# Kernel optimization log

Hardware: AMD Instinct MI355X
Metric: run time of the kernel (lower is better)

The kernel has to match this reference:

```python
import jax, jax.numpy as jnp
import numpy as np

E = 8        # n_routed_experts
TOPK = 2     # num_experts_per_tok


def setup_inputs() -> dict:
    key = jax.random.key(0)
    k0, k1, k2, k3, k4 = jax.random.split(key, 5)
    B, S, D, H = 1, 2048, 1024, 2816
    scale = 0.02
    x = jax.random.normal(k0, (B, S, D), jnp.float32)
    Wg = jax.random.normal(k1, (E, D), jnp.float32) * scale   # gate weight [E, D]
    W1 = jax.random.normal(k2, (E, H, D), jnp.float32) * scale  # up-gate proj
    W2 = jax.random.normal(k3, (E, D, H), jnp.float32) * scale  # down proj
    W3 = jax.random.normal(k4, (E, H, D), jnp.float32) * scale  # up proj
    return {"x": x, "Wg": Wg, "W1": W1, "W2": W2, "W3": W3}


def _moe_forward(x, Wg, W1, W2, W3):
    B, S, D = x.shape
    xt = x.reshape(-1, D)                      # [T, D], T = B*S
    T = xt.shape[0]
    # --- gate: logits -> softmax -> top-k, normalized top-k weights ---
    logits = xt @ Wg.T                         # [T, E]
    scores = jax.nn.softmax(logits, axis=-1)
    w, idx = jax.lax.top_k(scores, TOPK)       # [T, K]
    w = w / (w.sum(axis=-1, keepdims=True) + 1e-20)
    # combine weights per token per expert (scatter top-k weights) [T, E]
    cw = jnp.zeros((T, E), xt.dtype).at[jnp.arange(T)[:, None], idx].add(w)
    # --- per-expert SwiGLU FFN (batched over experts) ---
    h = jax.nn.silu(jnp.einsum('td,ehd->teh', xt, W1)) * jnp.einsum('td,ehd->teh', xt, W3)  # [T,E,H]
    out = jnp.einsum('teh,edh->ted', h, W2)    # [T, E, D]
    # weighted combine of selected experts (cw is zero for unselected)
    y = jnp.einsum('te,ted->td', cw, out)      # [T, D]
    return y.reshape(B, S, D)


def reference(x, Wg, W1, W2, W3):
    return _moe_forward(x, Wg, W1, W2, W3)
```

## Files before the change

kernel.cpp:

```cpp
#include <hip/hip_runtime.h>
#include <hip/hip_bf16.h>

#define T_TOK 2048
#define D_DIM 1024
#define H_DIM 2816
#define E_NUM 8
#define CAP   1024

typedef __attribute__((ext_vector_type(8))) short short8;
typedef __attribute__((ext_vector_type(4))) float floatx4;

__device__ __forceinline__ unsigned short f2bf(float f) {
    unsigned int b = __float_as_uint(f);
    b += 0x7FFFu + ((b >> 16) & 1u);
    return (unsigned short)(b >> 16);
}

__device__ __forceinline__ unsigned pk2(float lo, float hi) {
    unsigned a = __float_as_uint(lo) + 0x8000u;
    unsigned b = __float_as_uint(hi) + 0x8000u;
    return __builtin_amdgcn_perm(b, a, 0x07060302);
}

__device__ __forceinline__ short8 pack8r(float4 a, float4 b) {
    union { uint4 u; short8 s; } r;
    r.u.x = pk2(a.x, a.y);
    r.u.y = pk2(a.z, a.w);
    r.u.z = pk2(b.x, b.y);
    r.u.w = pk2(b.z, b.w);
    return r.s;
}

__device__ __forceinline__ void gl2lds16(const void* g, void* l) {
    __builtin_amdgcn_global_load_lds(
        (const __attribute__((address_space(1))) unsigned int*)g,
        (__attribute__((address_space(3))) unsigned int*)l,
        16, 0, 0);
}


__global__ __launch_bounds__(256) void k_gate2(const float* __restrict__ x,
                                               const float* __restrict__ Wg,
                                               int* __restrict__ stok,
                                               float* __restrict__ sw,
                                               int* __restrict__ counts,
                                               unsigned short* __restrict__ xg) {
    const int wave = threadIdx.x >> 6, lane = threadIdx.x & 63;
    const int t = blockIdx.x * 4 + wave;
    const float* xr = x + (size_t)t * D_DIM;
    float acc[E_NUM];
#pragma unroll
    for (int e = 0; e < E_NUM; ++e) acc[e] = 0.f;
#pragma unroll 4
    for (int i = 0; i < D_DIM / 64; ++i) {
        float xv = xr[lane + 64 * i];
#pragma unroll
        for (int e = 0; e < E_NUM; ++e) acc[e] += xv * Wg[e * D_DIM + lane + 64 * i];
    }
#pragma unroll
    for (int e = 0; e < E_NUM; ++e) {
#pragma unroll
        for (int s = 32; s > 0; s >>= 1) acc[e] += __shfl_xor(acc[e], s, 64);
    }
    int slot0 = 0, slot1 = 0;
    if (lane == 0) {
        float mx = acc[0];
#pragma unroll
        for (int e = 1; e < E_NUM; ++e) mx = fmaxf(mx, acc[e]);
        float p[E_NUM], s = 0.f;
#pragma unroll
        for (int e = 0; e < E_NUM; ++e) { p[e] = __expf(acc[e] - mx); s += p[e]; }
        int i0 = 0;
#pragma unroll
        for (int e = 1; e < E_NUM; ++e) if (p[e] > p[i0]) i0 = e;
        int i1 = (i0 == 0) ? 1 : 0;
#pragma unroll
        for (int e = 0; e < E_NUM; ++e) if (e != i0 && p[e] > p[i1]) i1 = e;
        float s0 = p[i0] / s, s1 = p[i1] / s;
        float d = s0 + s1 + 1e-20f;
        int p0 = atomicAdd(&counts[i0], 1); if (p0 >= CAP) p0 = CAP - 1;
        int p1 = atomicAdd(&counts[i1], 1); if (p1 >= CAP) p1 = CAP - 1;
        slot0 = i0 * CAP + p0;
        slot1 = i1 * CAP + p1;
        stok[slot0] = t; sw[slot0] = s0 / d;
        stok[slot1] = t; sw[slot1] = s1 / d;
    }
    slot0 = __shfl(slot0, 0, 64);
    slot1 = __shfl(slot1, 0, 64);
    const float4* xr4 = (const float4*)xr;
    ushort4* xg4 = (ushort4*)xg;
#pragma unroll
    for (int it = 0; it < 4; ++it) {
        float4 v = xr4[lane + 64 * it];
        ushort4 o;
        o.x = f2bf(v.x); o.y = f2bf(v.y); o.z = f2bf(v.z); o.w = f2bf(v.w);
        xg4[(size_t)slot0 * 256 + lane + 64 * it] = o;
        xg4[(size_t)slot1 * 256 + lane + 64 * it] = o;
    }
}

__global__ __launch_bounds__(256, 2) void k_gemm13(const unsigned short* __restrict__ xg,
                                                   const float* __restrict__ W1,
                                                   const float* __restrict__ W3,
                                                   const int* __restrict__ counts,
                                                   unsigned short* __restrict__ U) {
    const int nt = blockIdx.x;
    const int mt = blockIdx.y;
    const int e  = blockIdx.z;
    const int cnt = min(counts[e], CAP);
    if (mt * 256 >= cnt) return;

    __shared__ __align__(16) unsigned char As[32768];
    __shared__ __align__(16) unsigned char B1s[4096];
    __shared__ __align__(16) unsigned char B3s[4096];

    const int tid = threadIdx.x, lane = tid & 63, wave = tid >> 6;
    const int fr = lane & 15, quad = lane >> 4, f7 = fr & 7, f8 = fr >> 3;

    const unsigned short* aBase = xg
        + ((size_t)e * CAP + mt * 256 + wave * 64 + (lane >> 3)) * D_DIM
        + ((lane & 7) ^ (lane >> 3)) * 8;

    const int br = tid >> 3, bc = tid & 7;
    const float* w1p = W1 + ((size_t)e * H_DIM + nt * 32 + br) * D_DIM + bc * 8;
    const float* w3p = W3 + ((size_t)e * H_DIM + nt * 32 + br) * D_DIM + bc * 8;
    const int bslot = (br >> 3) * 1024 + (br & 7) * 128 + ((bc ^ (br & 7)) << 4);

    floatx4 acc1[4][2], acc3[4][2];
#pragma unroll
    for (int m = 0; m < 4; ++m)
#pragma unroll
        for (int n = 0; n < 2; ++n) { acc1[m][n] = (floatx4)0.f; acc3[m][n] = (floatx4)0.f; }

    const int agrp = (wave * 8 + f8) * 1024 + f7 * 128;
    const int c0 = (quad ^ f7) << 4;
    const int c1 = ((4 | quad) ^ f7) << 4;

#pragma unroll
    for (int j = 0; j < 8; ++j)
        gl2lds16(aBase + (size_t)j * 8 * D_DIM, As + (wave * 8 + j) * 1024);
    {
        float4 u0 = *(const float4*)(w1p);
        float4 u1 = *(const float4*)(w1p + 4);
        float4 v0 = *(const float4*)(w3p);
        float4 v1 = *(const float4*)(w3p + 4);
        *(short8*)(B1s + bslot) = pack8r(u0, u1);
        *(short8*)(B3s + bslot) = pack8r(v0, v1);
    }
    __syncthreads();

#pragma unroll 1
    for (int t = 0; t < D_DIM / 64; ++t) {
        short8 a[4][2], b1[2][2], b3[2][2];
#pragma unroll
        for (int m = 0; m < 4; ++m) {
            const unsigned char* ab = As + agrp + m * 2048;
            a[m][0] = *(const short8*)(ab + c0);
            a[m][1] = *(const short8*)(ab + c1);
        }
#pragma unroll
        for (int n = 0; n < 2; ++n) {
            const int bg = (n * 2 + f8) * 1024 + f7 * 128;
            b1[n][0] = *(const short8*)(B1s + bg + c0);
            b1[n][1] = *(const short8*)(B1s + bg + c1);
            b3[n][0] = *(const short8*)(B3s + bg + c0);
            b3[n][1] = *(const short8*)(B3s + bg + c1);
        }
        __syncthreads();

        const bool more = (t < D_DIM / 64 - 1);
        float4 u0, u1, v0, v1;
        if (more) {
            const int kn = (t + 1) * 64;
#pragma unroll
            for (int j = 0; j < 8; ++j)
                gl2lds16(aBase + (size_t)j * 8 * D_DIM + kn, As + (wave * 8 + j) * 1024);
            u0 = *(const float4*)(w1p + kn);
            u1 = *(const float4*)(w1p + kn + 4);
            v0 = *(const float4*)(w3p + kn);
            v1 = *(const float4*)(w3p + kn + 4);
        }

#pragma unroll
        for (int m = 0; m < 4; ++m) {
#pragma unroll
            for (int n = 0; n < 2; ++n) {
                acc1[m][n] = __builtin_amdgcn_mfma_f32_16x16x32_bf16(a[m][0], b1[n][0], acc1[m][n], 0, 0, 0);
                acc1[m][n] = __builtin_amdgcn_mfma_f32_16x16x32_bf16(a[m][1], b1[n][1], acc1[m][n], 0, 0, 0);
                acc3[m][n] = __builtin_amdgcn_mfma_f32_16x16x32_bf16(a[m][0], b3[n][0], acc3[m][n], 0, 0, 0);
                acc3[m][n] = __builtin_amdgcn_mfma_f32_16x16x32_bf16(a[m][1], b3[n][1], acc3[m][n], 0, 0, 0);
            }
        }

        if (more) {
            *(short8*)(B1s + bslot) = pack8r(u0, u1);
            *(short8*)(B3s + bslot) = pack8r(v0, v1);
            __syncthreads();
        }
    }

#pragma unroll
    for (int m = 0; m < 4; ++m) {
#pragma unroll
        for (int r = 0; r < 4; ++r) {
            int g = mt * 256 + wave * 64 + m * 16 + quad * 4 + r;
            if (g < cnt) {
                size_t rowb = ((size_t)e * CAP + g) * H_DIM + nt * 32;
#pragma unroll
                for (int n = 0; n < 2; ++n) {
                    float u1v = acc1[m][n][r], u3v = acc3[m][n][r];
                    float u = u1v / (1.f + __expf(-u1v)) * u3v;
                    U[rowb + n * 16 + fr] = f2bf(u);
                }
            }
        }
    }
}

__global__ __launch_bounds__(256, 2) void k_gemm2(const unsigned short* __restrict__ U,
                                                  const float* __restrict__ W2,
                                                  const int* __restrict__ counts,
                                                  const int* __restrict__ stok,
                                                  const float* __restrict__ sw,
                                                  float* __restrict__ y) {
    const int nt = blockIdx.x;
    const int mt = blockIdx.y;
    const int e  = blockIdx.z;
    const int cnt = min(counts[e], CAP);
    if (mt * 256 >= cnt) return;

    __shared__ __align__(16) unsigned char As[32768];
    __shared__ __align__(16) unsigned char Bs[8192];

    const int tid = threadIdx.x, lane = tid & 63, wave = tid >> 6;
    const int fr = lane & 15, quad = lane >> 4, f7 = fr & 7, f8 = fr >> 3;

    const unsigned short* aBase = U
        + ((size_t)e * CAP + mt * 256 + wave * 64 + (lane >> 3)) * H_DIM
        + ((lane & 7) ^ (lane >> 3)) * 8;

    const int br = tid >> 3, bc = tid & 7;
    const float* w2p0 = W2 + ((size_t)e * D_DIM + nt * 64 + br) * H_DIM + bc * 8;
    const float* w2p1 = w2p0 + (size_t)32 * H_DIM;
    const int bslot0 = (br >> 3) * 1024 + (br & 7) * 128 + ((bc ^ (br & 7)) << 4);
    const int bslot1 = bslot0 + 4096;

    floatx4 acc[4][4];
#pragma unroll
    for (int m = 0; m < 4; ++m)
#pragma unroll
        for (int n = 0; n < 4; ++n) acc[m][n] = (floatx4)0.f;

    const int agrp = (wave * 8 + f8) * 1024 + f7 * 128;
    const int c0 = (quad ^ f7) << 4;
    const int c1 = ((4 | quad) ^ f7) << 4;

#pragma unroll
    for (int j = 0; j < 8; ++j)
        gl2lds16(aBase + (size_t)j * 8 * H_DIM, As + (wave * 8 + j) * 1024);
    {
        float4 u0 = *(const float4*)(w2p0);
        float4 u1 = *(const float4*)(w2p0 + 4);
        float4 v0 = *(const float4*)(w2p1);
        float4 v1 = *(const float4*)(w2p1 + 4);
        *(short8*)(Bs + bslot0) = pack8r(u0, u1);
        *(short8*)(Bs + bslot1) = pack8r(v0, v1);
    }
    __syncthreads();

#pragma unroll 1
    for (int t = 0; t < H_DIM / 64; ++t) {
        short8 a[4][2], bf[4][2];
#pragma unroll
        for (int m = 0; m < 4; ++m) {
            const unsigned char* ab = As + agrp + m * 2048;
            a[m][0] = *(const short8*)(ab + c0);
            a[m][1] = *(const short8*)(ab + c1);
        }
#pragma unroll
        for (int n = 0; n < 4; ++n) {
            const int bg = (n * 2 + f8) * 1024 + f7 * 128;
            bf[n][0] = *(const short8*)(Bs + bg + c0);
            bf[n][1] = *(const short8*)(Bs + bg + c1);
        }
        __syncthreads();

        const bool more = (t < H_DIM / 64 - 1);
        float4 u0, u1, v0, v1;
        if (more) {
            const int kn = (t + 1) * 64;
#pragma unroll
            for (int j = 0; j < 8; ++j)
                gl2lds16(aBase + (size_t)j * 8 * H_DIM + kn, As + (wave * 8 + j) * 1024);
            u0 = *(const float4*)(w2p0 + kn);
            u1 = *(const float4*)(w2p0 + kn + 4);
            v0 = *(const float4*)(w2p1 + kn);
            v1 = *(const float4*)(w2p1 + kn + 4);
        }

#pragma unroll
        for (int m = 0; m < 4; ++m) {
#pragma unroll
            for (int n = 0; n < 4; ++n) {
                acc[m][n] = __builtin_amdgcn_mfma_f32_16x16x32_bf16(a[m][0], bf[n][0], acc[m][n], 0, 0, 0);
                acc[m][n] = __builtin_amdgcn_mfma_f32_16x16x32_bf16(a[m][1], bf[n][1], acc[m][n], 0, 0, 0);
            }
        }

        if (more) {
            *(short8*)(Bs + bslot0) = pack8r(u0, u1);
            *(short8*)(Bs + bslot1) = pack8r(v0, v1);
            __syncthreads();
        }
    }

#pragma unroll
    for (int m = 0; m < 4; ++m) {
#pragma unroll
        for (int r = 0; r < 4; ++r) {
            int g = mt * 256 + wave * 64 + m * 16 + quad * 4 + r;
            if (g < cnt) {
                int slot = e * CAP + g;
                int t = stok[slot];
                float w = sw[slot];
                float* yr = y + (size_t)t * D_DIM + nt * 64;
#pragma unroll
                for (int n = 0; n < 4; ++n)
                    atomicAdd(&yr[n * 16 + fr], w * acc[m][n][r]);
            }
        }
    }
}

static const size_t OFF_XG   = 0;
static const size_t OFF_U    = (size_t)E_NUM * CAP * D_DIM * 2;
static const size_t OFF_STOK = OFF_U + (size_t)E_NUM * CAP * H_DIM * 2;
static const size_t OFF_SW   = OFF_STOK + (size_t)E_NUM * CAP * 4;
static const size_t OFF_META = OFF_SW + (size_t)E_NUM * CAP * 4;

extern "C" void kernel_launch(void* const* d_in, const int* in_sizes, int n_in,
                              void* d_out, int out_size, void* d_ws, size_t ws_size,
                              hipStream_t stream) {
    const float* x  = (const float*)d_in[0];
    const float* Wg = (const float*)d_in[1];
    const float* W1 = (const float*)d_in[2];
    const float* W2 = (const float*)d_in[3];
    const float* W3 = (const float*)d_in[4];
    float* y = (float*)d_out;
    char* ws = (char*)d_ws;

    unsigned short* xg = (unsigned short*)(ws + OFF_XG);
    unsigned short* U  = (unsigned short*)(ws + OFF_U);
    int*   stok   = (int*)(ws + OFF_STOK);
    float* sw     = (float*)(ws + OFF_SW);
    int*   counts = (int*)(ws + OFF_META);

    hipMemsetAsync(counts, 0, 64, stream);
    hipMemsetAsync(y, 0, (size_t)T_TOK * D_DIM * sizeof(float), stream);

    k_gate2<<<T_TOK / 4, 256, 0, stream>>>(x, Wg, stok, sw, counts, xg);
    k_gemm13<<<dim3(H_DIM / 32, CAP / 256, E_NUM), 256, 0, stream>>>(xg, W1, W3, counts, U);
    k_gemm2<<<dim3(D_DIM / 64, CAP / 256, E_NUM), 256, 0, stream>>>(U, W2, counts, stok, sw, y);
}
```

Before: 431.2 us.

## Widen gate/up GEMM tile, split-K the down GEMM, reorder loads with sched barriers

The fused W1/W3 GEMM now computes 64 H-columns per block instead of 32, so each staged token tile is reused across twice as many output columns and the grid shrinks. The down-projection GEMM splits its H reduction into two halves across blocks, relying on the existing accumulate-into-y epilogue, to raise block count and parallelism. In both kernels the weight global loads for the next step are issued at the top of the iteration, fenced by sched_barrier, and the gemm13 MFMA work is split into two k-halves to overlap LDS reads with compute. The trade-offs are more accumulator registers and LDS in gemm13, which may hurt occupancy, and more atomic traffic to y from the split-K.

```diff
diff --git a/kernel.cpp b/kernel.cpp
--- a/kernel.cpp
+++ b/kernel.cpp
@@ -6,6 +6,9 @@
 #define H_DIM 2816
 #define E_NUM 8
 #define CAP   1024
+
+#define NT13  (D_DIM / 64)
+#define NT2H  (H_DIM / 128)
 
 typedef __attribute__((ext_vector_type(8))) short short8;
 typedef __attribute__((ext_vector_type(4))) float floatx4;
@@ -37,6 +40,8 @@
         (__attribute__((address_space(3))) unsigned int*)l,
         16, 0, 0);
 }
+
+#define SCHED0 __builtin_amdgcn_sched_barrier(0)
 
 
 __global__ __launch_bounds__(256) void k_gate2(const float* __restrict__ x,
@@ -111,8 +116,8 @@
     if (mt * 256 >= cnt) return;
 
     __shared__ __align__(16) unsigned char As[32768];
-    __shared__ __align__(16) unsigned char B1s[4096];
-    __shared__ __align__(16) unsigned char B3s[4096];
+    __shared__ __align__(16) unsigned char B1s[8192];
+    __shared__ __align__(16) unsigned char B3s[8192];
 
     const int tid = threadIdx.x, lane = tid & 63, wave = tid >> 6;
     const int fr = lane & 15, quad = lane >> 4, f7 = fr & 7, f8 = fr >> 3;
@@ -122,79 +127,111 @@
         + ((lane & 7) ^ (lane >> 3)) * 8;
 
     const int br = tid >> 3, bc = tid & 7;
-    const float* w1p = W1 + ((size_t)e * H_DIM + nt * 32 + br) * D_DIM + bc * 8;
-    const float* w3p = W3 + ((size_t)e * H_DIM + nt * 32 + br) * D_DIM + bc * 8;
+    const float* w1p = W1 + ((size_t)e * H_DIM + nt * 64 + br) * D_DIM + bc * 8;
+    const float* w3p = W3 + ((size_t)e * H_DIM + nt * 64 + br) * D_DIM + bc * 8;
     const int bslot = (br >> 3) * 1024 + (br & 7) * 128 + ((bc ^ (br & 7)) << 4);
 
-    floatx4 acc1[4][2], acc3[4][2];
+    floatx4 acc1[4][4], acc3[4][4];
 #pragma unroll
     for (int m = 0; m < 4; ++m)
 #pragma unroll
-        for (int n = 0; n < 2; ++n) { acc1[m][n] = (floatx4)0.f; acc3[m][n] = (floatx4)0.f; }
+        for (int n = 0; n < 4; ++n) { acc1[m][n] = (floatx4)0.f; acc3[m][n] = (floatx4)0.f; }
 
     const int agrp = (wave * 8 + f8) * 1024 + f7 * 128;
     const int c0 = (quad ^ f7) << 4;
     const int c1 = ((4 | quad) ^ f7) << 4;
 
-#pragma unroll
-    for (int j = 0; j < 8; ++j)
-        gl2lds16(aBase + (size_t)j * 8 * D_DIM, As + (wave * 8 + j) * 1024);
     {
         float4 u0 = *(const float4*)(w1p);
         float4 u1 = *(const float4*)(w1p + 4);
+        float4 u2 = *(const float4*)(w1p + (size_t)32 * D_DIM);
+        float4 u3 = *(const float4*)(w1p + (size_t)32 * D_DIM + 4);
         float4 v0 = *(const float4*)(w3p);
         float4 v1 = *(const float4*)(w3p + 4);
-        *(short8*)(B1s + bslot) = pack8r(u0, u1);
-        *(short8*)(B3s + bslot) = pack8r(v0, v1);
+        float4 v2 = *(const float4*)(w3p + (size_t)32 * D_DIM);
+        float4 v3 = *(const float4*)(w3p + (size_t)32 * D_DIM + 4);
+        SCHED0;
+#pragma unroll
+        for (int j = 0; j < 8; ++j)
+            gl2lds16(aBase + (size_t)j * 8 * D_DIM, As + (wave * 8 + j) * 1024);
+        SCHED0;
+        *(short8*)(B1s + bslot)        = pack8r(u0, u1);
+        *(short8*)(B1s + bslot + 4096) = pack8r(u2, u3);
+        *(short8*)(B3s + bslot)        = pack8r(v0, v1);
+        *(short8*)(B3s + bslot + 4096) = pack8r(v2, v3);
     }
     __syncthreads();
 
 #pragma unroll 1
-    for (int t = 0; t < D_DIM / 64; ++t) {
-        short8 a[4][2], b1[2][2], b3[2][2];
-#pragma unroll
-        for (int m = 0; m < 4; ++m) {
-            const unsigned char* ab = As + agrp + m * 2048;
-            a[m][0] = *(const short8*)(ab + c0);
-            a[m][1] = *(const short8*)(ab + c1);
-        }
-#pragma unroll
-        for (int n = 0; n < 2; ++n) {
+    for (int t = 0; t < NT13; ++t) {
+        const bool more = (t + 1 < NT13);
+        float4 u0, u1, u2, u3, v0, v1, v2, v3;
+        if (more) {
+            const int kn = (t + 1) * 64;
+            u0 = *(const float4*)(w1p + kn);
+            u1 = *(const float4*)(w1p + kn + 4);
+            u2 = *(const float4*)(w1p + (size_t)32 * D_DIM + kn);
+            u3 = *(const float4*)(w1p + (size_t)32 * D_DIM + kn + 4);
+            v0 = *(const float4*)(w3p + kn);
+            v1 = *(const float4*)(w3p + kn + 4);
+            v2 = *(const float4*)(w3p + (size_t)32 * D_DIM + kn);
+            v3 = *(const float4*)(w3p + (size_t)32 * D_DIM + kn + 4);
+        }
+        SCHED0;
+
+        {
+            short8 a[4], b1[4], b3[4];
+#pragma unroll
+            for (int m = 0; m < 4; ++m)
+                a[m] = *(const short8*)(As + agrp + m * 2048 + c0);
+#pragma unroll
+            for (int n = 0; n < 4; ++n) {
+                const int bg = (n * 2 + f8) * 1024 + f7 * 128;
+                b1[n] = *(const short8*)(B1s + bg + c0);
+                b3[n] = *(const short8*)(B3s + bg + c0);
+            }
+#pragma unroll
+            for (int m = 0; m < 4; ++m)
+#pragma unroll
+                for (int n = 0; n < 4; ++n) {
+                    acc1[m][n] = __builtin_amdgcn_mfma_f32_16x16x32_bf16(a[m], b1[n], acc1[m][n], 0, 0, 0);
+                    acc3[m][n] = __builtin_amdgcn_mfma_f32_16x16x32_bf16(a[m], b3[n], acc3[m][n], 0, 0, 0);
+                }
+        }
+
+        short8 a1[4], b11[4], b31[4];
+#pragma unroll
+        for (int m = 0; m < 4; ++m)
+            a1[m] = *(const short8*)(As + agrp + m * 2048 + c1);
+#pragma unroll
+        for (int n = 0; n < 4; ++n) {
             const int bg = (n * 2 + f8) * 1024 + f7 * 128;
-            b1[n][0] = *(const short8*)(B1s + bg + c0);
-            b1[n][1] = *(const short8*)(B1s + bg + c1);
-            b3[n][0] = *(const short8*)(B3s + bg + c0);
-            b3[n][1] = *(const short8*)(B3s + bg + c1);
+            b11[n] = *(const short8*)(B1s + bg + c1);
+            b31[n] = *(const short8*)(B3s + bg + c1);
         }
         __syncthreads();
 
-        const bool more = (t < D_DIM / 64 - 1);
-        float4 u0, u1, v0, v1;
         if (more) {
             const int kn = (t + 1) * 64;
 #pragma unroll
             for (int j = 0; j < 8; ++j)
                 gl2lds16(aBase + (size_t)j * 8 * D_DIM + kn, As + (wave * 8 + j) * 1024);
-            u0 = *(const float4*)(w1p + kn);
-            u1 = *(const float4*)(w1p + kn + 4);
-            v0 = *(const float4*)(w3p + kn);
-            v1 = *(const float4*)(w3p + kn + 4);
-        }
-
-#pragma unroll
-        for (int m = 0; m < 4; ++m) {
-#pragma unroll
-            for (int n = 0; n < 2; ++n) {
-                acc1[m][n] = __builtin_amdgcn_mfma_f32_16x16x32_bf16(a[m][0], b1[n][0], acc1[m][n], 0, 0, 0);
-                acc1[m][n] = __builtin_amdgcn_mfma_f32_16x16x32_bf16(a[m][1], b1[n][1], acc1[m][n], 0, 0, 0);
-                acc3[m][n] = __builtin_amdgcn_mfma_f32_16x16x32_bf16(a[m][0], b3[n][0], acc3[m][n], 0, 0, 0);
-                acc3[m][n] = __builtin_amdgcn_mfma_f32_16x16x32_bf16(a[m][1], b3[n][1], acc3[m][n], 0, 0, 0);
+        }
+        SCHED0;
+
+#pragma unroll
+        for (int m = 0; m < 4; ++m)
+#pragma unroll
+            for (int n = 0; n < 4; ++n) {
+                acc1[m][n] = __builtin_amdgcn_mfma_f32_16x16x32_bf16(a1[m], b11[n], acc1[m][n], 0, 0, 0);
+                acc3[m][n] = __builtin_amdgcn_mfma_f32_16x16x32_bf16(a1[m], b31[n], acc3[m][n], 0, 0, 0);
             }
-        }
-
-        if (more) {
-            *(short8*)(B1s + bslot) = pack8r(u0, u1);
-            *(short8*)(B3s + bslot) = pack8r(v0, v1);
+
+        if (more) {
+            *(short8*)(B1s + bslot)        = pack8r(u0, u1);
+            *(short8*)(B1s + bslot + 4096) = pack8r(u2, u3);
+            *(short8*)(B3s + bslot)        = pack8r(v0, v1);
+            *(short8*)(B3s + bslot + 4096) = pack8r(v2, v3);
             __syncthreads();
         }
     }
@@ -205,9 +242,9 @@
         for (int r = 0; r < 4; ++r) {
             int g = mt * 256 + wave * 64 + m * 16 + quad * 4 + r;
             if (g < cnt) {
-                size_t rowb = ((size_t)e * CAP + g) * H_DIM + nt * 32;
-#pragma unroll
-                for (int n = 0; n < 2; ++n) {
+                size_t rowb = ((size_t)e * CAP + g) * H_DIM + nt * 64;
+#pragma unroll
+                for (int n = 0; n < 4; ++n) {
                     float u1v = acc1[m][n][r], u3v = acc3[m][n][r];
                     float u = u1v / (1.f + __expf(-u1v)) * u3v;
                     U[rowb + n * 16 + fr] = f2bf(u);
@@ -223,7 +260,8 @@
                                                   const int* __restrict__ stok,
                                                   const float* __restrict__ sw,
                                                   float* __restrict__ y) {
-    const int nt = blockIdx.x;
+    const int nt = blockIdx.x >> 1;
+    const int kz = blockIdx.x & 1;
     const int mt = blockIdx.y;
     const int e  = blockIdx.z;
     const int cnt = min(counts[e], CAP);
@@ -234,13 +272,14 @@
 
     const int tid = threadIdx.x, lane = tid & 63, wave = tid >> 6;
     const int fr = lane & 15, quad = lane >> 4, f7 = fr & 7, f8 = fr >> 3;
+    const int kbase = kz * (H_DIM / 2);
 
     const unsigned short* aBase = U
         + ((size_t)e * CAP + mt * 256 + wave * 64 + (lane >> 3)) * H_DIM
-        + ((lane & 7) ^ (lane >> 3)) * 8;
+        + ((lane & 7) ^ (lane >> 3)) * 8 + kbase;
 
     const int br = tid >> 3, bc = tid & 7;
-    const float* w2p0 = W2 + ((size_t)e * D_DIM + nt * 64 + br) * H_DIM + bc * 8;
+    const float* w2p0 = W2 + ((size_t)e * D_DIM + nt * 64 + br) * H_DIM + bc * 8 + kbase;
     const float* w2p1 = w2p0 + (size_t)32 * H_DIM;
     const int bslot0 = (br >> 3) * 1024 + (br & 7) * 128 + ((bc ^ (br & 7)) << 4);
     const int bslot1 = bslot0 + 4096;
@@ -255,21 +294,34 @@
     const int c0 = (quad ^ f7) << 4;
     const int c1 = ((4 | quad) ^ f7) << 4;
 
-#pragma unroll
-    for (int j = 0; j < 8; ++j)
-        gl2lds16(aBase + (size_t)j * 8 * H_DIM, As + (wave * 8 + j) * 1024);
     {
         float4 u0 = *(const float4*)(w2p0);
         float4 u1 = *(const float4*)(w2p0 + 4);
         float4 v0 = *(const float4*)(w2p1);
         float4 v1 = *(const float4*)(w2p1 + 4);
+        SCHED0;
+#pragma unroll
+        for (int j = 0; j < 8; ++j)
+            gl2lds16(aBase + (size_t)j * 8 * H_DIM, As + (wave * 8 + j) * 1024);
+        SCHED0;
         *(short8*)(Bs + bslot0) = pack8r(u0, u1);
         *(short8*)(Bs + bslot1) = pack8r(v0, v1);
     }
     __syncthreads();
 
 #pragma unroll 1
-    for (int t = 0; t < H_DIM / 64; ++t) {
+    for (int t = 0; t < NT2H; ++t) {
+        const bool more = (t + 1 < NT2H);
+        float4 u0, u1, v0, v1;
+        if (more) {
+            const int kn = (t + 1) * 64;
+            u0 = *(const float4*)(w2p0 + kn);
+            u1 = *(const float4*)(w2p0 + kn + 4);
+            v0 = *(const float4*)(w2p1 + kn);
+            v1 = *(const float4*)(w2p1 + kn + 4);
+        }
+        SCHED0;
+
         short8 a[4][2], bf[4][2];
 #pragma unroll
         for (int m = 0; m < 4; ++m) {
@@ -285,27 +337,21 @@
         }
         __syncthreads();
 
-        const bool more = (t < H_DIM / 64 - 1);
-        float4 u0, u1, v0, v1;
         if (more) {
             const int kn = (t + 1) * 64;
 #pragma unroll
             for (int j = 0; j < 8; ++j)
                 gl2lds16(aBase + (size_t)j * 8 * H_DIM + kn, As + (wave * 8 + j) * 1024);
-            u0 = *(const float4*)(w2p0 + kn);
-            u1 = *(const float4*)(w2p0 + kn + 4);
-            v0 = *(const float4*)(w2p1 + kn);
-            v1 = *(const float4*)(w2p1 + kn + 4);
-        }
-
-#pragma unroll
-        for (int m = 0; m < 4; ++m) {
+        }
+        SCHED0;
+
+#pragma unroll
+        for (int m = 0; m < 4; ++m)
 #pragma unroll
             for (int n = 0; n < 4; ++n) {
                 acc[m][n] = __builtin_amdgcn_mfma_f32_16x16x32_bf16(a[m][0], bf[n][0], acc[m][n], 0, 0, 0);
                 acc[m][n] = __builtin_amdgcn_mfma_f32_16x16x32_bf16(a[m][1], bf[n][1], acc[m][n], 0, 0, 0);
             }
-        }
 
         if (more) {
             *(short8*)(Bs + bslot0) = pack8r(u0, u1);
@@ -359,6 +405,6 @@
     hipMemsetAsync(y, 0, (size_t)T_TOK * D_DIM * sizeof(float), stream);
 
     k_gate2<<<T_TOK / 4, 256, 0, stream>>>(x, Wg, stok, sw, counts, xg);
-    k_gemm13<<<dim3(H_DIM / 32, CAP / 256, E_NUM), 256, 0, stream>>>(xg, W1, W3, counts, U);
-    k_gemm2<<<dim3(D_DIM / 64, CAP / 256, E_NUM), 256, 0, stream>>>(U, W2, counts, stok, sw, y);
-}
+    k_gemm13<<<dim3(H_DIM / 64, CAP / 256, E_NUM), 256, 0, stream>>>(xg, W1, W3, counts, U);
+    k_gemm2<<<dim3(2 * D_DIM / 64, CAP / 256, E_NUM), 256, 0, stream>>>(U, W2, counts, stok, sw, y);
+}
```

New measurement: 411.5 us. -4.6%, faster.
